# Optimization experiments

Hardware: AMD Instinct MI355X
Metric: run time of the kernel (lower is better)

The kernel has to match this reference:

```python
import jax, jax.numpy as jnp
import numpy as np

N = 100000      # nodes
E = 3200000     # edges (avg degree 32)
F_IN = 128      # num_node_features
H = 16          # hidden dim (fixed in module)
C = 2           # num_classes


def setup_inputs() -> dict:
    key = jax.random.key(0)
    k0, k1, k2, k3 = jax.random.split(key, 4)
    x = jax.random.normal(k0, (N, F_IN), dtype=jnp.float32)
    edge_index = jax.random.randint(k1, (2, E), 0, N, dtype=jnp.int32)
    # GCNConv params: weight (in,out) + bias (out,) per layer (glorot-ish scale)
    W1 = jax.random.normal(k2, (F_IN, H), dtype=jnp.float32) * (1.0 / np.sqrt(F_IN))
    b1 = jnp.zeros((H,), jnp.float32)
    W2 = jax.random.normal(k3, (H, C), dtype=jnp.float32) * (1.0 / np.sqrt(H))
    b2 = jnp.zeros((C,), jnp.float32)
    return {"x": x, "edge_index": edge_index, "W1": W1, "b1": b1, "W2": W2, "b2": b2}


def _gcn_conv(x, W, b, src, dst, n):
    # GCNConv: h = D^{-1/2}(A+I)D^{-1/2} (x W) + b, with self-loops in src/dst
    h = x @ W                                   # [n, out]
    deg = jax.ops.segment_sum(jnp.ones_like(dst, dtype=h.dtype), dst, num_segments=n)
    dinv = jnp.where(deg > 0, jax.lax.rsqrt(deg), 0.0)
    norm = dinv[src] * dinv[dst]                # [E+n]
    msg = h[src] * norm[:, None]                # gather + scale
    out = jax.ops.segment_sum(msg, dst, num_segments=n)  # scatter-add
    return out + b


def reference(x, edge_index, W1, b1, W2, b2):
    loops = jnp.arange(N, dtype=edge_index.dtype)
    src = jnp.concatenate([edge_index[0], loops])
    dst = jnp.concatenate([edge_index[1], loops])
    h = jax.nn.relu(_gcn_conv(x, W1, b1, src, dst, N))
    # F.dropout(training=False) in eval mode is identity
    out = _gcn_conv(h, W2, b2, src, dst, N)
    return jax.nn.log_softmax(out, axis=1)
```

## Files before the change

kernel.cpp:

```cpp
#include <hip/hip_runtime.h>
#include <hip/hip_bf16.h>

#define NN 100000
#define NE 3200000
#define FIN 128
#define HD 16
#define CD 2

#define BSH 9
#define BSPAN 512
#define NBKT 196
#define CHUNK 8192
#define NPB ((NE + CHUNK - 1) / CHUNK)

__device__ __forceinline__ float bf2f(ushort u) {
    union { float f; unsigned int i; } v; v.i = ((unsigned int)u) << 16; return v.f;
}
__device__ __forceinline__ ushort f2b(float f) {
    union { float f; unsigned int u; } v; v.f = f;
    unsigned int r = (v.u + 0x7FFFu + ((v.u >> 16) & 1u)) >> 16;
    return (ushort)r;
}

__global__ __launch_bounds__(512) void k_cnt(const int* __restrict__ dst,
                                             int* __restrict__ cntmat) {
    __shared__ int h[NBKT];
    for (int i = threadIdx.x; i < NBKT; i += 512) h[i] = 0;
    __syncthreads();
    int cq = blockIdx.x * (CHUNK / 4);
    const int4* d4 = (const int4*)dst;
    #pragma unroll
    for (int j = 0; j < CHUNK / 2048; ++j) {
        int e4 = cq + j * 512 + threadIdx.x;
        if (e4 < NE / 4) {
            int4 d = d4[e4];
            atomicAdd(&h[d.x >> BSH], 1);
            atomicAdd(&h[d.y >> BSH], 1);
            atomicAdd(&h[d.z >> BSH], 1);
            atomicAdd(&h[d.w >> BSH], 1);
        }
    }
    __syncthreads();
    int* row = cntmat + (size_t)blockIdx.x * NBKT;
    for (int i = threadIdx.x; i < NBKT; i += 512) row[i] = h[i];
}

__global__ __launch_bounds__(512) void k_colscan(const int* __restrict__ cntmat,
                                                 int* __restrict__ relm,
                                                 int* __restrict__ btot) {
    __shared__ int sm[512];
    int j = blockIdx.x, t = threadIdx.x;
    int v = (t < NPB) ? cntmat[(size_t)t * NBKT + j] : 0;
    sm[t] = v;
    __syncthreads();
    for (int off = 1; off < 512; off <<= 1) {
        int u = 0;
        if (t >= off) u = sm[t - off];
        __syncthreads();
        if (t >= off) sm[t] += u;
        __syncthreads();
    }
    if (t < NPB) relm[(size_t)j * NPB + t] = t ? sm[t - 1] : 0;
    if (t == 511) btot[j] = sm[511];
}

__global__ __launch_bounds__(256) void k_scanb(const int* __restrict__ btot,
                                               int* __restrict__ boff) {
    __shared__ int sm[256];
    int t = threadIdx.x;
    sm[t] = (t < NBKT) ? btot[t] : 0;
    __syncthreads();
    for (int off = 1; off < 256; off <<= 1) {
        int v = 0;
        if (t >= off) v = sm[t - off];
        __syncthreads();
        if (t >= off) sm[t] += v;
        __syncthreads();
    }
    if (t < NBKT) boff[t] = t ? sm[t - 1] : 0;
    if (t == 255) boff[NBKT] = sm[255];
}

__global__ __launch_bounds__(512) void k_part(const int* __restrict__ src,
                                              const int* __restrict__ dst,
                                              const int* __restrict__ boff,
                                              const int* __restrict__ relm,
                                              unsigned int* __restrict__ csrb) {
    __shared__ int cur[NBKT];
    int b = blockIdx.x, t = threadIdx.x;
    for (int i = t; i < NBKT; i += 512)
        cur[i] = boff[i] + relm[(size_t)i * NPB + b];
    __syncthreads();
    int cq = b * (CHUNK / 4);
    const int4* s4 = (const int4*)src;
    const int4* d4 = (const int4*)dst;
    #pragma unroll
    for (int j = 0; j < CHUNK / 2048; ++j) {
        int e4 = cq + j * 512 + t;
        if (e4 < NE / 4) {
            int4 s = s4[e4];
            int4 d = d4[e4];
            int p;
            p = atomicAdd(&cur[d.x >> BSH], 1);
            csrb[p] = (unsigned)s.x | ((unsigned)(d.x & (BSPAN - 1)) << 17);
            p = atomicAdd(&cur[d.y >> BSH], 1);
            csrb[p] = (unsigned)s.y | ((unsigned)(d.y & (BSPAN - 1)) << 17);
            p = atomicAdd(&cur[d.z >> BSH], 1);
            csrb[p] = (unsigned)s.z | ((unsigned)(d.z & (BSPAN - 1)) << 17);
            p = atomicAdd(&cur[d.w >> BSH], 1);
            csrb[p] = (unsigned)s.w | ((unsigned)(d.w & (BSPAN - 1)) << 17);
        }
    }
}

__global__ __launch_bounds__(512) void k_dg(const int* __restrict__ boff,
                                            const unsigned int* __restrict__ csrb,
                                            const float* __restrict__ x,
                                            const float* __restrict__ W1,
                                            int* __restrict__ csr2,
                                            int* __restrict__ rowptr,
                                            float* __restrict__ dinv,
                                            ushort* __restrict__ h1b) {
    __shared__ float wsm[FIN][HD];
    __shared__ int cnt[BSPAN];
    __shared__ int sc[BSPAN];
    __shared__ int cur[BSPAN];
    __shared__ float sdv[BSPAN];
    int b = blockIdx.x, t = threadIdx.x;
    for (int i = t; i < FIN * HD; i += 512) wsm[i >> 4][i & 15] = W1[i];
    cnt[t] = 0;
    __syncthreads();
    int e0 = boff[b], e1 = boff[b + 1];
    for (int e = e0 + t; e < e1; e += 512) atomicAdd(&cnt[csrb[e] >> 17], 1);
    __syncthreads();
    sc[t] = cnt[t];
    __syncthreads();
    for (int off = 1; off < BSPAN; off <<= 1) {
        int v = 0;
        if (t >= off) v = sc[t - off];
        __syncthreads();
        if (t >= off) sc[t] += v;
        __syncthreads();
    }
    {
        int ex = e0 + (t ? sc[t - 1] : 0);
        cur[t] = ex;
        float di = rsqrtf((float)cnt[t] + 1.0f);
        sdv[t] = di;
        int node = b * BSPAN + t;
        if (node < NN) {
            rowptr[node] = ex;
            dinv[node] = di;
        }
    }
    if (b == 0 && t == 0) rowptr[NN] = boff[NBKT];
    __syncthreads();
    for (int e = e0 + t; e < e1; e += 512) {
        unsigned p = csrb[e];
        int pos = atomicAdd(&cur[p >> 17], 1);
        csr2[pos] = (int)(p & 0x1FFFF);
    }
    #pragma unroll
    for (int it = 0; it < 4; ++it) {
        int task = it * 512 + t;
        int nl = task >> 2;
        int node = b * BSPAN + nl;
        if (node >= NN) break;
        int g = (task & 3) * 4;
        const float4* xr = (const float4*)(x + (size_t)node * FIN);
        float a0 = 0.f, a1 = 0.f, a2 = 0.f, a3 = 0.f;
        #pragma unroll
        for (int k4 = 0; k4 < FIN / 4; ++k4) {
            float4 v = xr[k4];
            #pragma unroll
            for (int kk = 0; kk < 4; ++kk) {
                float vk = (kk == 0) ? v.x : (kk == 1) ? v.y : (kk == 2) ? v.z : v.w;
                float4 w = *(const float4*)&wsm[k4 * 4 + kk][g];
                a0 += vk * w.x;
                a1 += vk * w.y;
                a2 += vk * w.z;
                a3 += vk * w.w;
            }
        }
        float di = sdv[nl];
        ushort4 r = {f2b(a0 * di), f2b(a1 * di), f2b(a2 * di), f2b(a3 * di)};
        *(ushort4*)(h1b + (size_t)node * HD + g) = r;
    }
}

__global__ __launch_bounds__(256) void k_agg1(const int* __restrict__ rowptr,
                                              const int* __restrict__ csr2,
                                              const ushort* __restrict__ h1b,
                                              const float* __restrict__ dinv,
                                              const float* __restrict__ b1,
                                              const float* __restrict__ W2,
                                              float* __restrict__ g_s) {
    int wid = (blockIdx.x * 256 + threadIdx.x) >> 6;
    int lane = threadIdx.x & 63;
    int node = wid * 4 + (lane >> 4);
    if (node >= NN) return;
    int l16 = lane & 15;
    int slot = l16 >> 2;
    int fq = (lane & 3) * 4;
    int e0 = rowptr[node], e1 = rowptr[node + 1];
    float a0 = 0.f, a1 = 0.f, a2 = 0.f, a3 = 0.f;
    float c0 = 0.f, c1 = 0.f, c2 = 0.f, c3 = 0.f;
    int e = e0 + slot;
    for (; e + 4 < e1; e += 8) {
        int s0 = csr2[e];
        int s1 = csr2[e + 4];
        ushort4 u0 = *(const ushort4*)(h1b + (size_t)s0 * HD + fq);
        ushort4 u1 = *(const ushort4*)(h1b + (size_t)s1 * HD + fq);
        a0 += bf2f(u0.x); a1 += bf2f(u0.y); a2 += bf2f(u0.z); a3 += bf2f(u0.w);
        c0 += bf2f(u1.x); c1 += bf2f(u1.y); c2 += bf2f(u1.z); c3 += bf2f(u1.w);
    }
    if (e < e1) {
        ushort4 u = *(const ushort4*)(h1b + (size_t)csr2[e] * HD + fq);
        a0 += bf2f(u.x); a1 += bf2f(u.y); a2 += bf2f(u.z); a3 += bf2f(u.w);
    }
    a0 += c0; a1 += c1; a2 += c2; a3 += c3;
    #pragma unroll
    for (int m = 4; m <= 8; m <<= 1) {
        a0 += __shfl_xor(a0, m, 64);
        a1 += __shfl_xor(a1, m, 64);
        a2 += __shfl_xor(a2, m, 64);
        a3 += __shfl_xor(a3, m, 64);
    }
    if (slot == 0) {
        float di = dinv[node];
        ushort4 us = *(const ushort4*)(h1b + (size_t)node * HD + fq);
        float v0 = fmaxf(di * (a0 + bf2f(us.x)) + b1[fq],     0.f);
        float v1 = fmaxf(di * (a1 + bf2f(us.y)) + b1[fq + 1], 0.f);
        float v2 = fmaxf(di * (a2 + bf2f(us.z)) + b1[fq + 2], 0.f);
        float v3 = fmaxf(di * (a3 + bf2f(us.w)) + b1[fq + 3], 0.f);
        float p0 = v0 * W2[fq * 2]       + v1 * W2[(fq + 1) * 2]
                 + v2 * W2[(fq + 2) * 2] + v3 * W2[(fq + 3) * 2];
        float p1 = v0 * W2[fq * 2 + 1]       + v1 * W2[(fq + 1) * 2 + 1]
                 + v2 * W2[(fq + 2) * 2 + 1] + v3 * W2[(fq + 3) * 2 + 1];
        p0 += __shfl_xor(p0, 1, 64); p0 += __shfl_xor(p0, 2, 64);
        p1 += __shfl_xor(p1, 1, 64); p1 += __shfl_xor(p1, 2, 64);
        if (l16 == 0) {
            float2 r = {p0 * di, p1 * di};
            *(float2*)(g_s + (size_t)node * 2) = r;
        }
    }
}

__global__ __launch_bounds__(256) void k_agg2(const int* __restrict__ rowptr,
                                              const int* __restrict__ csr2,
                                              const float* __restrict__ g_s,
                                              const float* __restrict__ dinv,
                                              const float* __restrict__ b2,
                                              float* __restrict__ out) {
    int wid = (blockIdx.x * 256 + threadIdx.x) >> 6;
    int lane = threadIdx.x & 63;
    int node = wid * 4 + (lane >> 4);
    if (node >= NN) return;
    int l16 = lane & 15;
    int slot = l16 >> 1, f = lane & 1;
    int e0 = rowptr[node], e1 = rowptr[node + 1];
    float acc = 0.f;
    for (int e = e0 + slot; e < e1; e += 8)
        acc += g_s[(size_t)csr2[e] * 2 + f];
    #pragma unroll
    for (int m = 2; m <= 8; m <<= 1) acc += __shfl_xor(acc, m, 64);
    if (slot == 0) {
        float di = dinv[node];
        float o = di * (acc + g_s[(size_t)node * 2 + f]) + b2[f];
        float other = __shfl_xor(o, 1, 64);
        float mx = fmaxf(o, other);
        float l = mx + logf(__expf(o - mx) + __expf(other - mx));
        out[(size_t)node * 2 + f] = o - l;
    }
}

extern "C" void kernel_launch(void* const* d_in, const int* in_sizes, int n_in,
                              void* d_out, int out_size, void* d_ws, size_t ws_size,
                              hipStream_t stream) {
    const float* x   = (const float*)d_in[0];
    const int* ei    = (const int*)d_in[1];
    const int* src   = ei;
    const int* dst   = ei + NE;
    const float* W1  = (const float*)d_in[2];
    const float* b1  = (const float*)d_in[3];
    const float* W2  = (const float*)d_in[4];
    const float* b2  = (const float*)d_in[5];
    float* out = (float*)d_out;

    char* w = (char*)d_ws;
    float* dinv        = (float*)w;          w += NN * 4;
    int*   btot        = (int*)w;            w += NBKT * 4;
    int*   boff        = (int*)w;            w += (NBKT + 1) * 4;
    int*   rowptr      = (int*)w;            w += (NN + 1) * 4;
    int*   cntmat      = (int*)w;            w += (size_t)NPB * NBKT * 4;
    int*   relm        = (int*)w;            w += (size_t)NBKT * NPB * 4;
    unsigned int* csrb = (unsigned int*)w;   w += (size_t)NE * 4;
    int*   csr2        = (int*)w;            w += (size_t)NE * 4;
    ushort* h1b        = (ushort*)w;         w += (size_t)NN * HD * 2;
    float* g_s         = (float*)w;          w += NN * CD * 4;

    k_cnt    <<<NPB, 512, 0, stream>>>(dst, cntmat);
    k_colscan<<<NBKT, 512, 0, stream>>>(cntmat, relm, btot);
    k_scanb  <<<1, 256, 0, stream>>>(btot, boff);
    k_part   <<<NPB, 512, 0, stream>>>(src, dst, boff, relm, csrb);
    k_dg     <<<NBKT, 512, 0, stream>>>(boff, csrb, x, W1, csr2, rowptr, dinv, h1b);
    k_agg1   <<<(NN * 16 + 255) / 256, 256, 0, stream>>>(rowptr, csr2, h1b, dinv, b1, W2, g_s);
    k_agg2   <<<(NN * 16 + 255) / 256, 256, 0, stream>>>(rowptr, csr2, g_s, dinv, b2, out);
}
```

Before: 219.1 us.

## Move x@W1 into the edge-count kernel and fold bucket scan into consumers

```diff
diff --git a/kernel.cpp b/kernel.cpp
--- a/kernel.cpp
+++ b/kernel.cpp
@@ -22,27 +22,59 @@
     return (ushort)r;
 }
 
-__global__ __launch_bounds__(512) void k_cnt(const int* __restrict__ dst,
-                                             int* __restrict__ cntmat) {
+__global__ __launch_bounds__(512) void k_head(const int* __restrict__ dst,
+                                              const float* __restrict__ x,
+                                              const float* __restrict__ W1,
+                                              int* __restrict__ cntmat,
+                                              ushort* __restrict__ h1b) {
+    __shared__ float wsm[FIN][HD];
     __shared__ int h[NBKT];
-    for (int i = threadIdx.x; i < NBKT; i += 512) h[i] = 0;
-    __syncthreads();
-    int cq = blockIdx.x * (CHUNK / 4);
-    const int4* d4 = (const int4*)dst;
-    #pragma unroll
-    for (int j = 0; j < CHUNK / 2048; ++j) {
-        int e4 = cq + j * 512 + threadIdx.x;
-        if (e4 < NE / 4) {
-            int4 d = d4[e4];
-            atomicAdd(&h[d.x >> BSH], 1);
-            atomicAdd(&h[d.y >> BSH], 1);
-            atomicAdd(&h[d.z >> BSH], 1);
-            atomicAdd(&h[d.w >> BSH], 1);
-        }
-    }
-    __syncthreads();
-    int* row = cntmat + (size_t)blockIdx.x * NBKT;
-    for (int i = threadIdx.x; i < NBKT; i += 512) row[i] = h[i];
+    int b = blockIdx.x, t = threadIdx.x;
+    for (int i = t; i < FIN * HD; i += 512) wsm[i >> 4][i & 15] = W1[i];
+    for (int i = t; i < NBKT; i += 512) h[i] = 0;
+    __syncthreads();
+    if (b < NPB) {
+        int cq = b * (CHUNK / 4);
+        const int4* d4 = (const int4*)dst;
+        #pragma unroll
+        for (int j = 0; j < CHUNK / 2048; ++j) {
+            int e4 = cq + j * 512 + t;
+            if (e4 < NE / 4) {
+                int4 d = d4[e4];
+                atomicAdd(&h[d.x >> BSH], 1);
+                atomicAdd(&h[d.y >> BSH], 1);
+                atomicAdd(&h[d.z >> BSH], 1);
+                atomicAdd(&h[d.w >> BSH], 1);
+            }
+        }
+    }
+    int task = b * 512 + t;
+    if (task < NN * 4) {
+        int node = task >> 2;
+        int g = (task & 3) * 4;
+        const float4* xr = (const float4*)(x + (size_t)node * FIN);
+        float a0 = 0.f, a1 = 0.f, a2 = 0.f, a3 = 0.f;
+        #pragma unroll
+        for (int k4 = 0; k4 < FIN / 4; ++k4) {
+            float4 v = xr[k4];
+            #pragma unroll
+            for (int kk = 0; kk < 4; ++kk) {
+                float vk = (kk == 0) ? v.x : (kk == 1) ? v.y : (kk == 2) ? v.z : v.w;
+                float4 w = *(const float4*)&wsm[k4 * 4 + kk][g];
+                a0 += vk * w.x;
+                a1 += vk * w.y;
+                a2 += vk * w.z;
+                a3 += vk * w.w;
+            }
+        }
+        ushort4 r = {f2b(a0), f2b(a1), f2b(a2), f2b(a3)};
+        *(ushort4*)(h1b + (size_t)node * HD + g) = r;
+    }
+    if (b < NPB) {
+        __syncthreads();
+        int* row = cntmat + (size_t)b * NBKT;
+        for (int i = t; i < NBKT; i += 512) row[i] = h[i];
+    }
 }
 
 __global__ __launch_bounds__(512) void k_colscan(const int* __restrict__ cntmat,
@@ -64,32 +96,25 @@
     if (t == 511) btot[j] = sm[511];
 }
 
-__global__ __launch_bounds__(256) void k_scanb(const int* __restrict__ btot,
-                                               int* __restrict__ boff) {
-    __shared__ int sm[256];
-    int t = threadIdx.x;
-    sm[t] = (t < NBKT) ? btot[t] : 0;
-    __syncthreads();
-    for (int off = 1; off < 256; off <<= 1) {
-        int v = 0;
-        if (t >= off) v = sm[t - off];
-        __syncthreads();
-        if (t >= off) sm[t] += v;
-        __syncthreads();
-    }
-    if (t < NBKT) boff[t] = t ? sm[t - 1] : 0;
-    if (t == 255) boff[NBKT] = sm[255];
-}
-
 __global__ __launch_bounds__(512) void k_part(const int* __restrict__ src,
                                               const int* __restrict__ dst,
-                                              const int* __restrict__ boff,
+                                              const int* __restrict__ btot,
                                               const int* __restrict__ relm,
                                               unsigned int* __restrict__ csrb) {
+    __shared__ int sb[256];
     __shared__ int cur[NBKT];
     int b = blockIdx.x, t = threadIdx.x;
+    if (t < 256) sb[t] = (t < NBKT) ? btot[t] : 0;
+    __syncthreads();
+    for (int off = 1; off < 256; off <<= 1) {
+        int u = 0;
+        if (t < 256 && t >= off) u = sb[t - off];
+        __syncthreads();
+        if (t < 256 && t >= off) sb[t] += u;
+        __syncthreads();
+    }
     for (int i = t; i < NBKT; i += 512)
-        cur[i] = boff[i] + relm[(size_t)i * NPB + b];
+        cur[i] = (i ? sb[i - 1] : 0) + relm[(size_t)i * NPB + b];
     __syncthreads();
     int cq = b * (CHUNK / 4);
     const int4* s4 = (const int4*)src;
@@ -113,24 +138,31 @@
     }
 }
 
-__global__ __launch_bounds__(512) void k_dg(const int* __restrict__ boff,
-                                            const unsigned int* __restrict__ csrb,
-                                            const float* __restrict__ x,
-                                            const float* __restrict__ W1,
-                                            int* __restrict__ csr2,
-                                            int* __restrict__ rowptr,
-                                            float* __restrict__ dinv,
-                                            ushort* __restrict__ h1b) {
-    __shared__ float wsm[FIN][HD];
+__global__ __launch_bounds__(512) void k_sorts(const int* __restrict__ btot,
+                                               const unsigned int* __restrict__ csrb,
+                                               int* __restrict__ csr2,
+                                               int* __restrict__ rowptr,
+                                               float* __restrict__ dinv,
+                                               ushort* __restrict__ h1b) {
+    __shared__ int sb[256];
     __shared__ int cnt[BSPAN];
     __shared__ int sc[BSPAN];
     __shared__ int cur[BSPAN];
     __shared__ float sdv[BSPAN];
     int b = blockIdx.x, t = threadIdx.x;
-    for (int i = t; i < FIN * HD; i += 512) wsm[i >> 4][i & 15] = W1[i];
+    if (t < 256) sb[t] = (t < NBKT) ? btot[t] : 0;
     cnt[t] = 0;
     __syncthreads();
-    int e0 = boff[b], e1 = boff[b + 1];
+    for (int off = 1; off < 256; off <<= 1) {
+        int u = 0;
+        if (t < 256 && t >= off) u = sb[t - off];
+        __syncthreads();
+        if (t < 256 && t >= off) sb[t] += u;
+        __syncthreads();
+    }
+    int e0 = b ? sb[b - 1] : 0;
+    int e1 = sb[b];
+    __syncthreads();
     for (int e = e0 + t; e < e1; e += 512) atomicAdd(&cnt[csrb[e] >> 17], 1);
     __syncthreads();
     sc[t] = cnt[t];
@@ -153,38 +185,28 @@
             dinv[node] = di;
         }
     }
-    if (b == 0 && t == 0) rowptr[NN] = boff[NBKT];
+    if (b == 0 && t == 0) rowptr[NN] = NE;
     __syncthreads();
     for (int e = e0 + t; e < e1; e += 512) {
         unsigned p = csrb[e];
         int pos = atomicAdd(&cur[p >> 17], 1);
         csr2[pos] = (int)(p & 0x1FFFF);
     }
-    #pragma unroll
-    for (int it = 0; it < 4; ++it) {
-        int task = it * 512 + t;
-        int nl = task >> 2;
-        int node = b * BSPAN + nl;
-        if (node >= NN) break;
-        int g = (task & 3) * 4;
-        const float4* xr = (const float4*)(x + (size_t)node * FIN);
-        float a0 = 0.f, a1 = 0.f, a2 = 0.f, a3 = 0.f;
-        #pragma unroll
-        for (int k4 = 0; k4 < FIN / 4; ++k4) {
-            float4 v = xr[k4];
+    {
+        int node = b * BSPAN + t;
+        if (node < NN) {
+            float di = sdv[t];
+            ushort4* hp = (ushort4*)(h1b + (size_t)node * HD);
             #pragma unroll
-            for (int kk = 0; kk < 4; ++kk) {
-                float vk = (kk == 0) ? v.x : (kk == 1) ? v.y : (kk == 2) ? v.z : v.w;
-                float4 w = *(const float4*)&wsm[k4 * 4 + kk][g];
-                a0 += vk * w.x;
-                a1 += vk * w.y;
-                a2 += vk * w.z;
-                a3 += vk * w.w;
+            for (int j = 0; j < 4; ++j) {
+                ushort4 u = hp[j];
+                u.x = f2b(bf2f(u.x) * di);
+                u.y = f2b(bf2f(u.y) * di);
+                u.z = f2b(bf2f(u.z) * di);
+                u.w = f2b(bf2f(u.w) * di);
+                hp[j] = u;
             }
         }
-        float di = sdv[nl];
-        ushort4 r = {f2b(a0 * di), f2b(a1 * di), f2b(a2 * di), f2b(a3 * di)};
-        *(ushort4*)(h1b + (size_t)node * HD + g) = r;
     }
 }
 
@@ -290,7 +312,6 @@
     char* w = (char*)d_ws;
     float* dinv        = (float*)w;          w += NN * 4;
     int*   btot        = (int*)w;            w += NBKT * 4;
-    int*   boff        = (int*)w;            w += (NBKT + 1) * 4;
     int*   rowptr      = (int*)w;            w += (NN + 1) * 4;
     int*   cntmat      = (int*)w;            w += (size_t)NPB * NBKT * 4;
     int*   relm        = (int*)w;            w += (size_t)NBKT * NPB * 4;
@@ -299,11 +320,10 @@
     ushort* h1b        = (ushort*)w;         w += (size_t)NN * HD * 2;
     float* g_s         = (float*)w;          w += NN * CD * 4;
 
-    k_cnt    <<<NPB, 512, 0, stream>>>(dst, cntmat);
+    k_head   <<<(NN * 4 + 511) / 512, 512, 0, stream>>>(dst, x, W1, cntmat, h1b);
     k_colscan<<<NBKT, 512, 0, stream>>>(cntmat, relm, btot);
-    k_scanb  <<<1, 256, 0, stream>>>(btot, boff);
-    k_part   <<<NPB, 512, 0, stream>>>(src, dst, boff, relm, csrb);
-    k_dg     <<<NBKT, 512, 0, stream>>>(boff, csrb, x, W1, csr2, rowptr, dinv, h1b);
+    k_part   <<<NPB, 512, 0, stream>>>(src, dst, btot, relm, csrb);
+    k_sorts  <<<NBKT, 512, 0, stream>>>(btot, csrb, csr2, rowptr, dinv, h1b);
     k_agg1   <<<(NN * 16 + 255) / 256, 256, 0, stream>>>(rowptr, csr2, h1b, dinv, b1, W2, g_s);
     k_agg2   <<<(NN * 16 + 255) / 256, 256, 0, stream>>>(rowptr, csr2, g_s, dinv, b2, out);
 }
```

Result: no change. 220.7 us (+0.8%).
